# Kernel tuning notes

Measured on AMD Instinct MI355X. Metric: run time of the kernel, lower is better.

Reference implementation:

```python
import jax, jax.numpy as jnp
import numpy as np

B, H, N, D = 2, 8, 2048, 64


def setup_inputs() -> dict:
    key = jax.random.key(0)
    kq, kk, kv = jax.random.split(key, 3)
    q = jax.random.normal(kq, (B, H, N, D), dtype=jnp.float32)
    k = jax.random.normal(kk, (B, H, N, D), dtype=jnp.float32)
    v = jax.random.normal(kv, (B, H, N, D), dtype=jnp.float32)
    return {"q": q, "k": k, "v": v}


def _selective_attn(sim):
    # sim: (b, h, i, j). Gate computed from first head, relu'd, SOS unmasked,
    # diagonal zeroed, shifted down one row, cumsum over query rows, subtracted.
    b, h, i, j = sim.shape
    gate = jax.nn.relu(sim[:, 0])                       # (b, i, j)
    gate = gate.at[:, :, j - i].set(0.0)                # no_mask_sos: column -i
    eye = jnp.eye(i, dtype=sim.dtype)
    if j > i:
        eye = jnp.pad(eye, ((0, 0), (j - i, 0)), constant_values=1.0)
    gate = (1.0 - eye) * gate
    # F.pad(gate, (0,0,1,-1)): shift rows down by one, drop last row
    gate = jnp.pad(gate, ((0, 0), (1, 0), (0, 0)))[:, :i, :]
    gate = jnp.cumsum(gate, axis=-2)
    return sim - gate[:, None]                          # broadcast over heads


def reference(q, k, v):
    scale = q.shape[-1] ** -0.5
    i, j = q.shape[-2], k.shape[-2]

    # squared L2 distance scores: ||q||^2 + ||k||^2 - 2 q.k  (== cdist(q,k)**2)
    q_sq = jnp.sum(q * q, axis=-1)                      # (b, h, i)
    k_sq = jnp.sum(k * k, axis=-1)                      # (b, h, j)
    qk = jnp.einsum('bhid,bhjd->bhij', q, k)            # (b, h, i, j)
    d2 = jnp.maximum(q_sq[..., :, None] + k_sq[..., None, :] - 2.0 * qk, 0.0)
    sim = -d2 * scale

    # causal mask (triu with offset j - i + 1)
    mask_value = -jnp.finfo(sim.dtype).max
    causal = jnp.triu(jnp.ones((i, j), dtype=bool), j - i + 1)
    sim = jnp.where(causal, mask_value, sim)

    # selective attention gating
    sim = _selective_attn(sim)

    # one-hot straight-through attention
    idx = jnp.argmax(sim, axis=-1)                      # (b, h, i)
    hard = jax.nn.one_hot(idx, j, dtype=sim.dtype)      # (b, h, i, j)
    soft = jax.nn.softmax(sim, axis=-1)
    attn = hard + soft - jax.lax.stop_gradient(soft)

    return jnp.einsum('bhij,bhjd->bhid', attn, v)
```

## Files before the change

### kernel.cpp

```cpp
#include <hip/hip_runtime.h>
#include <stdint.h>

#define B_ 2
#define H_ 8
#define N_ 2048
#define D_ 64
#define BH_ (B_ * H_)
#define NROWS (BH_ * N_)
#define TPB_ 288
#define TASKS (TPB_ * BH_)
#define EPSF 8e-3f
#define INFF __int_as_float(0x7f800000)

using u64 = unsigned long long;
using u32 = unsigned int;
typedef __attribute__((ext_vector_type(8))) short short8;
typedef __attribute__((ext_vector_type(4))) float f32x4;

#define MFMA16(A, B, C) __builtin_amdgcn_mfma_f32_16x16x32_bf16((A), (B), (C), 0, 0, 0)

__global__ __launch_bounds__(256) void prep_k(
    const float* __restrict__ k, char* __restrict__ khi_g,
    char* __restrict__ klo_g, float* __restrict__ ksq_g,
    u32* __restrict__ count)
{
  if (blockIdx.x == 0 && threadIdx.x == 0) count[0] = 0;
  const int t = (int)blockIdx.x * 256 + threadIdx.x;
  const int r = t >> 3, kg = t & 7;
  const float* kp = k + (size_t)r * D_ + kg * 8;
  const float4 f0 = *(const float4*)kp;
  const float4 f1 = *(const float4*)(kp + 4);
  const float vv[8] = {f0.x, f0.y, f0.z, f0.w, f1.x, f1.y, f1.z, f1.w};
  u32 hw[4], lw[4];
  float ps = 0.f;
  #pragma unroll
  for (int e = 0; e < 4; ++e) {
    const float va = vv[2 * e], vb = vv[2 * e + 1];
    ps = fmaf(va, va, ps); ps = fmaf(vb, vb, ps);
    const u32 ha = __float_as_uint(va) & 0xFFFF0000u;
    const u32 hb = __float_as_uint(vb) & 0xFFFF0000u;
    hw[e] = (ha >> 16) | hb;
    const u32 la = __float_as_uint(va - __uint_as_float(ha));
    const u32 lb = __float_as_uint(vb - __uint_as_float(hb));
    lw[e] = (la >> 16) | (lb & 0xFFFF0000u);
  }
  const size_t off = ((size_t)(r >> 4) * 2 + (kg >> 2)) * 1024 +
                     (size_t)(((kg & 3) << 4) + (r & 15)) * 16;
  *(uint4*)(khi_g + off) = make_uint4(hw[0], hw[1], hw[2], hw[3]);
  *(uint4*)(klo_g + off) = make_uint4(lw[0], lw[1], lw[2], lw[3]);
  float ssum = ps;
  ssum += __shfl_xor(ssum, 1);
  ssum += __shfl_xor(ssum, 2);
  ssum += __shfl_xor(ssum, 4);
  if (kg == 0) ksq_g[r] = ssum;
}

__device__ __forceinline__ void cvt_hilo(const float* p, short8& hi, short8& lo) {
  const float4 f0 = *(const float4*)p;
  const float4 f1 = *(const float4*)(p + 4);
  const float vv[8] = {f0.x, f0.y, f0.z, f0.w, f1.x, f1.y, f1.z, f1.w};
  #pragma unroll
  for (int e = 0; e < 8; ++e) {
    const float v = vv[e];
    const u32 hb = __float_as_uint(v) & 0xFFFF0000u;
    hi[e] = (short)(hb >> 16);
    lo[e] = (short)(__float_as_uint(v - __uint_as_float(hb)) >> 16);
  }
}

__global__ __launch_bounds__(64, 3) void phase1(
    const float* __restrict__ q, const char* __restrict__ khi_g,
    const char* __restrict__ klo_g, const float* __restrict__ ksq_g,
    u64* __restrict__ bestc, u32* __restrict__ secc)
{
  const int b = (int)blockIdx.x;
  const int task = (b & 7) * (TASKS / 8) + (b >> 3);
  const int bh = task / TPB_;
  int rem = task - bh * TPB_;
  int g2 = 0, nc = 1;
  while (rem >= nc) { rem -= nc; ++g2; nc = (2 * g2 + 17) >> 4; }
  const int c = rem;
  const int jfirst = c * 16;
  const int jlast = min(jfirst + 15, 2 * g2 + 1);

  const int lane = threadIdx.x & 63;
  const int grp = lane >> 4, c0 = lane & 15;
  const int i0 = g2 * 32;

  short8 ah00, ah01, al00, al01, ah10, ah11, al10, al11;
  {
    const float* q0 = q + ((size_t)bh * N_ + i0 + c0) * D_ + grp * 8;
    cvt_hilo(q0, ah00, al00);
    cvt_hilo(q0 + 32, ah01, al01);
    const float* q1 = q0 + 16 * D_;
    cvt_hilo(q1, ah10, al10);
    cvt_hilo(q1 + 32, ah11, al11);
  }

  float bf[2][4], sf[2][4];
  u32 bj[2][4];
  #pragma unroll
  for (int s = 0; s < 2; ++s)
    #pragma unroll
    for (int r2 = 0; r2 < 4; ++r2) {
      bf[s][r2] = INFF; sf[s][r2] = INFF; bj[s][r2] = 0;
    }

  const size_t fb = (size_t)bh * 128 * 2048;
  const char* ph = khi_g + fb + (size_t)jfirst * 2048 + lane * 16;
  const char* pl = klo_g + fb + (size_t)jfirst * 2048 + lane * 16;
  const float* pk = ksq_g + (size_t)bh * N_ + jfirst * 16 + c0;

  for (int js = jfirst; js <= jlast; ++js) {
    const short8 ch0 = *(const short8*)(ph);
    const short8 ch1 = *(const short8*)(ph + 1024);
    const short8 cl0 = *(const short8*)(pl);
    const short8 cl1 = *(const short8*)(pl + 1024);
    const float cks = *pk;
    ph += 2048; pl += 2048; pk += 16;

    const int jcol = js * 16 + c0;
    if (js <= 2 * g2) {
      const bool dsub = (js == 2 * g2);
      f32x4 aA = {0.f, 0.f, 0.f, 0.f}, aB = {0.f, 0.f, 0.f, 0.f};
      aA = MFMA16(ah00, ch0, aA);  aB = MFMA16(ah01, ch1, aB);
      aA = MFMA16(ah00, cl0, aA);  aB = MFMA16(ah01, cl1, aB);
      aA = MFMA16(al00, ch0, aA);  aB = MFMA16(al01, ch1, aB);
      #pragma unroll
      for (int reg = 0; reg < 4; ++reg) {
        float score = fmaf(-2.f, aA[reg] + aB[reg], cks);
        if (dsub && jcol > i0 + grp * 4 + reg) score = INFF;
        const float loser = fmaxf(bf[0][reg], score);
        sf[0][reg] = fminf(sf[0][reg], loser);
        if (score < bf[0][reg]) bj[0][reg] = (u32)jcol;
        bf[0][reg] = fminf(bf[0][reg], score);
      }
    }
    {
      const bool dsub = (js == 2 * g2 + 1);
      f32x4 aA = {0.f, 0.f, 0.f, 0.f}, aB = {0.f, 0.f, 0.f, 0.f};
      aA = MFMA16(ah10, ch0, aA);  aB = MFMA16(ah11, ch1, aB);
      aA = MFMA16(ah10, cl0, aA);  aB = MFMA16(ah11, cl1, aB);
      aA = MFMA16(al10, ch0, aA);  aB = MFMA16(al11, ch1, aB);
      #pragma unroll
      for (int reg = 0; reg < 4; ++reg) {
        float score = fmaf(-2.f, aA[reg] + aB[reg], cks);
        if (dsub && jcol > i0 + 16 + grp * 4 + reg) score = INFF;
        const float loser = fmaxf(bf[1][reg], score);
        sf[1][reg] = fminf(sf[1][reg], loser);
        if (score < bf[1][reg]) bj[1][reg] = (u32)jcol;
        bf[1][reg] = fminf(bf[1][reg], score);
      }
    }
  }

  #pragma unroll
  for (int s = 0; s < 2; ++s) {
    #pragma unroll
    for (int reg = 0; reg < 4; ++reg) {
      const u32 bbits = __float_as_uint(bf[s][reg]);
      const u32 key = bbits ^ (u32)(((int)bbits >> 31) | 0x80000000);
      u64 pkk = ((u64)key << 32) | bj[s][reg];
      float sv = sf[s][reg];
      #pragma unroll
      for (int m = 1; m < 16; m <<= 1) {
        const u64 opk = (u64)__shfl_xor((long long)pkk, m);
        const float osv = __shfl_xor(sv, m);
        const u32 mk = (u32)(pkk >> 32), ok = (u32)(opk >> 32);
        const u32 lk = (opk < pkk) ? mk : ok;
        const u32 lb = (lk & 0x80000000u) ? (lk ^ 0x80000000u) : ~lk;
        sv = fminf(fminf(sv, osv), __uint_as_float(lb));
        if (opk < pkk) pkk = opk;
      }
      if (c0 == 0) {
        const size_t rr = (size_t)bh * N_ + i0 + s * 16 + grp * 4 + reg;
        bestc[(size_t)c * NROWS + rr] = pkk;
        secc[(size_t)c * NROWS + rr] = __float_as_uint(sv);
      }
    }
  }
}

__global__ __launch_bounds__(256) void combine_gather(
    const u64* __restrict__ bestc, const u32* __restrict__ secc,
    const float* __restrict__ v, float* __restrict__ out,
    u32* __restrict__ flaglist, u32* __restrict__ count)
{
  __shared__ u64 pk_s[4][64];
  __shared__ float s1_s[4][64];
  __shared__ u32 idx_s[64];
  const int tid = threadIdx.x;
  const int r0 = (int)blockIdx.x * 64;
  const int p = tid >> 6, t6 = tid & 63;

  {
    const int r = r0 + t6;
    const int i = r & (N_ - 1);
    const int nch = (2 * (i >> 5) + 17) >> 4;
    u64 b0 = ~0ull;
    float bcur = INFF, s1 = INFF;
    int cstar = -1;
    for (int c2 = p; c2 < nch; c2 += 4) {
      const u64 kk = bestc[(size_t)c2 * NROWS + r];
      const u32 key = (u32)(kk >> 32);
      const u32 bits = (key & 0x80000000u) ? (key ^ 0x80000000u) : ~key;
      const float f = __uint_as_float(bits);
      if (kk < b0) { s1 = fminf(s1, bcur); b0 = kk; bcur = f; cstar = c2; }
      else s1 = fminf(s1, f);
    }
    if (cstar >= 0)
      s1 = fminf(s1, __uint_as_float(secc[(size_t)cstar * NROWS + r]));
    pk_s[p][t6] = b0;
    s1_s[p][t6] = s1;
  }
  __syncthreads();

  if (tid < 64) {
    u64 b0 = ~0ull;
    float bcur = INFF, s1 = INFF;
    #pragma unroll
    for (int pp = 0; pp < 4; ++pp) {
      const u64 kk = pk_s[pp][tid];
      const u32 key = (u32)(kk >> 32);
      const u32 bits = (key & 0x80000000u) ? (key ^ 0x80000000u) : ~key;
      const float f = __uint_as_float(bits);
      if (kk < b0) { s1 = fminf(s1, bcur); b0 = kk; bcur = f; }
      else s1 = fminf(s1, f);
      s1 = fminf(s1, s1_s[pp][tid]);
    }
    idx_s[tid] = (u32)(b0 & 0xFFFFu);
    if ((s1 - bcur) < EPSF) {
      const u32 pos = atomicAdd(count, 1u);
      flaglist[pos] = (u32)(r0 + tid);
    }
  }
  __syncthreads();

  #pragma unroll
  for (int iter = 0; iter < 4; ++iter) {
    const int tk = tid + iter * 256;
    const int rl = tk >> 4, cc = tk & 15;
    const int r = r0 + rl;
    const u32 j = idx_s[rl];
    const int bh = r >> 11;
    const float4 val = ((const float4*)(v + ((size_t)bh * N_ + j) * D_))[cc];
    ((float4*)(out + (size_t)r * D_))[cc] = val;
  }
}

__global__ __launch_bounds__(64) void exact_partial(
    const float* __restrict__ q, const float* __restrict__ k,
    const u32* __restrict__ flaglist, const u32* __restrict__ count,
    double* __restrict__ pd, int* __restrict__ pj)
{
  const int lane = threadIdx.x & 63;
  const int cnt = (int)count[0];
  for (int t = blockIdx.x; (t >> 4) < cnt; t += (int)gridDim.x) {
    const int li = t >> 4, slice = t & 15;
    const int r = (int)flaglist[li];
    const int bh = r >> 11;
    const int i = r & (N_ - 1);
    const int jbase = slice * 128;

    double bbest = 1e300;
    int bjj = 0x7FFFFFFF;
    if (jbase <= i) {
      const float4* qr = (const float4*)(q + (size_t)r * D_);
      float4 qv[16];
      #pragma unroll
      for (int t2 = 0; t2 < 16; ++t2) qv[t2] = qr[t2];
      double s0 = 0, s1 = 0, s2 = 0, s3 = 0;
      #pragma unroll
      for (int t2 = 0; t2 < 16; ++t2) {
        s0 = fma((double)qv[t2].x, (double)qv[t2].x, s0);
        s1 = fma((double)qv[t2].y, (double)qv[t2].y, s1);
        s2 = fma((double)qv[t2].z, (double)qv[t2].z, s2);
        s3 = fma((double)qv[t2].w, (double)qv[t2].w, s3);
      }
      const double qsqd = (s0 + s1) + (s2 + s3);
      const float* kb = k + (size_t)bh * N_ * D_;

      #pragma unroll
      for (int u = 0; u < 2; ++u) {
        const int j = jbase + u * 64 + lane;
        if (j <= i) {
          const float4* kr = (const float4*)(kb + (size_t)j * D_);
          double a0 = 0, a1 = 0, a2 = 0, a3 = 0;
          double t0 = 0, t1 = 0, t2d = 0, t3 = 0;
          #pragma unroll
          for (int t2 = 0; t2 < 16; ++t2) {
            const float4 kv = kr[t2];
            const double k0 = kv.x, k1 = kv.y, k2 = kv.z, k3 = kv.w;
            a0 = fma((double)qv[t2].x, k0, a0);
            a1 = fma((double)qv[t2].y, k1, a1);
            a2 = fma((double)qv[t2].z, k2, a2);
            a3 = fma((double)qv[t2].w, k3, a3);
            t0 = fma(k0, k0, t0);
            t1 = fma(k1, k1, t1);
            t2d = fma(k2, k2, t2d);
            t3 = fma(k3, k3, t3);
          }
          const double raw = (qsqd + ((t0 + t1) + (t2d + t3))) -
                             2.0 * ((a0 + a1) + (a2 + a3));
          const double d2 = raw > 0.0 ? raw : 0.0;
          if (d2 < bbest) { bbest = d2; bjj = j; }
        }
      }
      #pragma unroll
      for (int m = 1; m < 64; m <<= 1) {
        const double ob = __shfl_xor(bbest, m);
        const int oj = __shfl_xor(bjj, m);
        if (ob < bbest || (ob == bbest && oj < bjj)) { bbest = ob; bjj = oj; }
      }
    }
    if (lane == 0) {
      pd[(size_t)li * 16 + slice] = bbest;
      pj[(size_t)li * 16 + slice] = bjj;
    }
  }
}

__global__ __launch_bounds__(64) void exact_final(
    const double* __restrict__ pd, const int* __restrict__ pj,
    const u32* __restrict__ flaglist, const u32* __restrict__ count,
    const float* __restrict__ v, float* __restrict__ out)
{
  const int lane = threadIdx.x & 63;
  const int cnt = (int)count[0];
  for (int li = blockIdx.x; li < cnt; li += (int)gridDim.x) {
    const int r = (int)flaglist[li];
    const int bh = r >> 11;
    double d = (lane < 16) ? pd[(size_t)li * 16 + lane] : 1e300;
    int j = (lane < 16) ? pj[(size_t)li * 16 + lane] : 0x7FFFFFFF;
    #pragma unroll
    for (int m = 1; m < 16; m <<= 1) {
      const double od = __shfl_xor(d, m);
      const int oj = __shfl_xor(j, m);
      if (od < d || (od == d && oj < j)) { d = od; j = oj; }
    }
    if (lane < 16) {
      const float4 val =
          ((const float4*)(v + ((size_t)bh * N_ + j) * D_))[lane];
      ((float4*)(out + (size_t)r * D_))[lane] = val;
    }
  }
}

extern "C" void kernel_launch(void* const* d_in, const int* in_sizes, int n_in,
                              void* d_out, int out_size, void* d_ws,
                              size_t ws_size, hipStream_t stream) {
  const float* q = (const float*)d_in[0];
  const float* k = (const float*)d_in[1];
  const float* v = (const float*)d_in[2];
  float* out = (float*)d_out;

  char* ws = (char*)d_ws;
  u32* count = (u32*)ws;
  u32* flaglist = (u32*)(ws + 4096);
  float* ksq_g = (float*)(ws + 256 * 1024);
  char* khi_g = ws + 1ull * 1024 * 1024;
  char* klo_g = ws + 8ull * 1024 * 1024;
  u64* bestc = (u64*)(ws + 16ull * 1024 * 1024);
  u32* secc = (u32*)(ws + 24ull * 1024 * 1024);
  double* pd = (double*)(ws + 32ull * 1024 * 1024);
  int* pj = (int*)(ws + 40ull * 1024 * 1024);

  prep_k<<<(NROWS * 8) / 256, 256, 0, stream>>>(k, khi_g, klo_g, ksq_g, count);
  phase1<<<TASKS, 64, 0, stream>>>(q, khi_g, klo_g, ksq_g, bestc, secc);
  combine_gather<<<NROWS / 64, 256, 0, stream>>>(bestc, secc, v, out,
                                                 flaglist, count);
  exact_partial<<<2048, 64, 0, stream>>>(q, k, flaglist, count, pd, pj);
  exact_final<<<256, 64, 0, stream>>>(pd, pj, flaglist, count, v, out);
}
```

Before: 56.54 us.

## Shrink phase1 row tiles to 16 rows for finer causal work split

Phase1 now gives each wavefront one 16-row query tile instead of two, doubling the task count per head (576). A closed-form mapping from task to (row group, chunk) replaces the loop walk, and the occupancy hint goes from 3 to 6. The aim is to trim causal triangle waste and raise occupancy and load balance. In exchange, each K tile loaded from global memory is reused across half as many query rows, so K traffic roughly doubles.

```diff
diff --git a/kernel.cpp b/kernel.cpp
--- a/kernel.cpp
+++ b/kernel.cpp
@@ -7,7 +7,7 @@
 #define D_ 64
 #define BH_ (B_ * H_)
 #define NROWS (BH_ * N_)
-#define TPB_ 288
+#define TPB_ 576
 #define TASKS (TPB_ * BH_)
 #define EPSF 8e-3f
 #define INFF __int_as_float(0x7f800000)
@@ -68,7 +68,7 @@
   }
 }
 
-__global__ __launch_bounds__(64, 3) void phase1(
+__global__ __launch_bounds__(64, 6) void phase1(
     const float* __restrict__ q, const char* __restrict__ khi_g,
     const char* __restrict__ klo_g, const float* __restrict__ ksq_g,
     u64* __restrict__ bestc, u32* __restrict__ secc)
@@ -76,35 +76,33 @@
   const int b = (int)blockIdx.x;
   const int task = (b & 7) * (TASKS / 8) + (b >> 3);
   const int bh = task / TPB_;
-  int rem = task - bh * TPB_;
-  int g2 = 0, nc = 1;
-  while (rem >= nc) { rem -= nc; ++g2; nc = (2 * g2 + 17) >> 4; }
-  const int c = rem;
+  const int rem = task - bh * TPB_;
+  int m = 0;
+  while (8 * (m + 1) * (m + 2) <= rem) ++m;
+  const int idx = rem - 8 * m * (m + 1);
+  const int qn = idx / (m + 1);
+  const int g1 = 16 * m + qn;
+  const int c = idx - qn * (m + 1);
   const int jfirst = c * 16;
-  const int jlast = min(jfirst + 15, 2 * g2 + 1);
+  const int jlast = min(jfirst + 15, g1);
 
   const int lane = threadIdx.x & 63;
   const int grp = lane >> 4, c0 = lane & 15;
-  const int i0 = g2 * 32;
-
-  short8 ah00, ah01, al00, al01, ah10, ah11, al10, al11;
+  const int i0 = g1 * 16;
+
+  short8 ah0, ah1, al0, al1;
   {
     const float* q0 = q + ((size_t)bh * N_ + i0 + c0) * D_ + grp * 8;
-    cvt_hilo(q0, ah00, al00);
-    cvt_hilo(q0 + 32, ah01, al01);
-    const float* q1 = q0 + 16 * D_;
-    cvt_hilo(q1, ah10, al10);
-    cvt_hilo(q1 + 32, ah11, al11);
-  }
-
-  float bf[2][4], sf[2][4];
-  u32 bj[2][4];
-  #pragma unroll
-  for (int s = 0; s < 2; ++s)
-    #pragma unroll
-    for (int r2 = 0; r2 < 4; ++r2) {
-      bf[s][r2] = INFF; sf[s][r2] = INFF; bj[s][r2] = 0;
-    }
+    cvt_hilo(q0, ah0, al0);
+    cvt_hilo(q0 + 32, ah1, al1);
+  }
+
+  float bf[4], sf[4];
+  u32 bj[4];
+  #pragma unroll
+  for (int r2 = 0; r2 < 4; ++r2) {
+    bf[r2] = INFF; sf[r2] = INFF; bj[r2] = 0;
+  }
 
   const size_t fb = (size_t)bh * 128 * 2048;
   const char* ph = khi_g + fb + (size_t)jfirst * 2048 + lane * 16;
@@ -120,63 +118,42 @@
     ph += 2048; pl += 2048; pk += 16;
 
     const int jcol = js * 16 + c0;
-    if (js <= 2 * g2) {
-      const bool dsub = (js == 2 * g2);
-      f32x4 aA = {0.f, 0.f, 0.f, 0.f}, aB = {0.f, 0.f, 0.f, 0.f};
-      aA = MFMA16(ah00, ch0, aA);  aB = MFMA16(ah01, ch1, aB);
-      aA = MFMA16(ah00, cl0, aA);  aB = MFMA16(ah01, cl1, aB);
-      aA = MFMA16(al00, ch0, aA);  aB = MFMA16(al01, ch1, aB);
-      #pragma unroll
-      for (int reg = 0; reg < 4; ++reg) {
-        float score = fmaf(-2.f, aA[reg] + aB[reg], cks);
-        if (dsub && jcol > i0 + grp * 4 + reg) score = INFF;
-        const float loser = fmaxf(bf[0][reg], score);
-        sf[0][reg] = fminf(sf[0][reg], loser);
-        if (score < bf[0][reg]) bj[0][reg] = (u32)jcol;
-        bf[0][reg] = fminf(bf[0][reg], score);
-      }
-    }
-    {
-      const bool dsub = (js == 2 * g2 + 1);
-      f32x4 aA = {0.f, 0.f, 0.f, 0.f}, aB = {0.f, 0.f, 0.f, 0.f};
-      aA = MFMA16(ah10, ch0, aA);  aB = MFMA16(ah11, ch1, aB);
-      aA = MFMA16(ah10, cl0, aA);  aB = MFMA16(ah11, cl1, aB);
-      aA = MFMA16(al10, ch0, aA);  aB = MFMA16(al11, ch1, aB);
-      #pragma unroll
-      for (int reg = 0; reg < 4; ++reg) {
-        float score = fmaf(-2.f, aA[reg] + aB[reg], cks);
-        if (dsub && jcol > i0 + 16 + grp * 4 + reg) score = INFF;
-        const float loser = fmaxf(bf[1][reg], score);
-        sf[1][reg] = fminf(sf[1][reg], loser);
-        if (score < bf[1][reg]) bj[1][reg] = (u32)jcol;
-        bf[1][reg] = fminf(bf[1][reg], score);
-      }
-    }
-  }
-
-  #pragma unroll
-  for (int s = 0; s < 2; ++s) {
+    const bool dsub = (js == g1);
+    f32x4 aA = {0.f, 0.f, 0.f, 0.f}, aB = {0.f, 0.f, 0.f, 0.f};
+    aA = MFMA16(ah0, ch0, aA);  aB = MFMA16(ah1, ch1, aB);
+    aA = MFMA16(ah0, cl0, aA);  aB = MFMA16(ah1, cl1, aB);
+    aA = MFMA16(al0, ch0, aA);  aB = MFMA16(al1, ch1, aB);
     #pragma unroll
     for (int reg = 0; reg < 4; ++reg) {
-      const u32 bbits = __float_as_uint(bf[s][reg]);
-      const u32 key = bbits ^ (u32)(((int)bbits >> 31) | 0x80000000);
-      u64 pkk = ((u64)key << 32) | bj[s][reg];
-      float sv = sf[s][reg];
-      #pragma unroll
-      for (int m = 1; m < 16; m <<= 1) {
-        const u64 opk = (u64)__shfl_xor((long long)pkk, m);
-        const float osv = __shfl_xor(sv, m);
-        const u32 mk = (u32)(pkk >> 32), ok = (u32)(opk >> 32);
-        const u32 lk = (opk < pkk) ? mk : ok;
-        const u32 lb = (lk & 0x80000000u) ? (lk ^ 0x80000000u) : ~lk;
-        sv = fminf(fminf(sv, osv), __uint_as_float(lb));
-        if (opk < pkk) pkk = opk;
-      }
-      if (c0 == 0) {
-        const size_t rr = (size_t)bh * N_ + i0 + s * 16 + grp * 4 + reg;
-        bestc[(size_t)c * NROWS + rr] = pkk;
-        secc[(size_t)c * NROWS + rr] = __float_as_uint(sv);
-      }
+      float score = fmaf(-2.f, aA[reg] + aB[reg], cks);
+      if (dsub && jcol > i0 + grp * 4 + reg) score = INFF;
+      const float loser = fmaxf(bf[reg], score);
+      sf[reg] = fminf(sf[reg], loser);
+      if (score < bf[reg]) bj[reg] = (u32)jcol;
+      bf[reg] = fminf(bf[reg], score);
+    }
+  }
+
+  #pragma unroll
+  for (int reg = 0; reg < 4; ++reg) {
+    const u32 bbits = __float_as_uint(bf[reg]);
+    const u32 key = bbits ^ (u32)(((int)bbits >> 31) | 0x80000000);
+    u64 pkk = ((u64)key << 32) | bj[reg];
+    float sv = sf[reg];
+    #pragma unroll
+    for (int mm = 1; mm < 16; mm <<= 1) {
+      const u64 opk = (u64)__shfl_xor((long long)pkk, mm);
+      const float osv = __shfl_xor(sv, mm);
+      const u32 mk = (u32)(pkk >> 32), ok = (u32)(opk >> 32);
+      const u32 lk = (opk < pkk) ? mk : ok;
+      const u32 lb = (lk & 0x80000000u) ? (lk ^ 0x80000000u) : ~lk;
+      sv = fminf(fminf(sv, osv), __uint_as_float(lb));
+      if (opk < pkk) pkk = opk;
+    }
+    if (c0 == 0) {
+      const size_t rr = (size_t)bh * N_ + i0 + grp * 4 + reg;
+      bestc[(size_t)c * NROWS + rr] = pkk;
+      secc[(size_t)c * NROWS + rr] = __float_as_uint(sv);
     }
   }
 }
@@ -196,7 +173,7 @@
   {
     const int r = r0 + t6;
     const int i = r & (N_ - 1);
-    const int nch = (2 * (i >> 5) + 17) >> 4;
+    const int nch = ((i >> 4) + 16) >> 4;
     u64 b0 = ~0ull;
     float bcur = INFF, s1 = INFF;
     int cstar = -1;
@@ -307,9 +284,9 @@
         }
       }
       #pragma unroll
-      for (int m = 1; m < 64; m <<= 1) {
-        const double ob = __shfl_xor(bbest, m);
-        const int oj = __shfl_xor(bjj, m);
+      for (int mm = 1; mm < 64; mm <<= 1) {
+        const double ob = __shfl_xor(bbest, mm);
+        const int oj = __shfl_xor(bjj, mm);
         if (ob < bbest || (ob == bbest && oj < bjj)) { bbest = ob; bjj = oj; }
       }
     }
@@ -333,9 +310,9 @@
     double d = (lane < 16) ? pd[(size_t)li * 16 + lane] : 1e300;
     int j = (lane < 16) ? pj[(size_t)li * 16 + lane] : 0x7FFFFFFF;
     #pragma unroll
-    for (int m = 1; m < 16; m <<= 1) {
-      const double od = __shfl_xor(d, m);
-      const int oj = __shfl_xor(j, m);
+    for (int mm = 1; mm < 16; mm <<= 1) {
+      const double od = __shfl_xor(d, mm);
+      const int oj = __shfl_xor(j, mm);
       if (od < d || (od == d && oj < j)) { d = od; j = oj; }
     }
     if (lane < 16) {
```

Measured after the change: 54.12 us, median of 2. 4.3% less time.
